# Performance work log

Measured on AMD Instinct MI355X. Metric: run time of the kernel, lower is better.

## Reference

```python
import jax, jax.numpy as jnp
import numpy as np
import math

EPS = 1e-6
N_HEADS = 16
THETA = 10000.0


def rms(x):
    # parameter-free RMSNorm: x * rsqrt(mean(x^2) + eps)
    return x * jax.lax.rsqrt(jnp.mean(x * x, axis=-1, keepdims=True) + EPS)


def silu(x):
    return x * jax.nn.sigmoid(x)


def rope_cos_sin(T, head_dim, theta):
    inv = 1.0 / (theta ** (jnp.arange(0, head_dim, 2, dtype=jnp.float32) / head_dim))
    freqs = jnp.arange(T, dtype=jnp.float32)[:, None] * inv[None, :]  # (T, head_dim/2)
    return jnp.cos(freqs), jnp.sin(freqs)


def apply_rope(x, cos, sin):
    # x: (B, H, T, dh); even/odd interleaved pairs as in torch reshape(...,-1,2).unbind(-1)
    x1 = x[..., 0::2]
    x2 = x[..., 1::2]
    o1 = x1 * cos - x2 * sin
    o2 = x1 * sin + x2 * cos
    return jnp.stack([o1, o2], axis=-1).reshape(x.shape)


def cache_linear(x, down, up):
    # x: (B,T,in), down: (h,in,c), up: (h,out,c) -> (B,T,out)
    a = jnp.einsum('bti,hic->bthc', x, down)
    a = jnp.einsum('bthc,hoc->btho', a, up)
    return rms(jnp.prod(a, axis=2))


def setup_inputs() -> dict:
    key = jax.random.key(0)
    ks = jax.random.split(key, 10)
    B, T, D = 1, 2048, 1024
    d_ff, ncb, cdim = 4096, 4, 64
    lin_std = math.sqrt(2.0 / (D + D))
    return {
        'x': jax.random.normal(ks[0], (B, T, D), jnp.float32),
        'ln1_w': jnp.ones((D,), jnp.float32),
        'ln2_w': jnp.ones((D,), jnp.float32),
        'wq': jax.random.normal(ks[1], (D, D), jnp.float32) * lin_std,
        'wk': jax.random.normal(ks[2], (D, D), jnp.float32) * lin_std,
        'wv': jax.random.normal(ks[3], (D, D), jnp.float32) * lin_std,
        'wo': jax.random.normal(ks[4], (D, D), jnp.float32) * lin_std,
        'w1_down': jax.random.normal(ks[5], (ncb, D, cdim), jnp.float32) * math.sqrt(2.0 / (D + cdim)),
        'w1_up': jax.random.normal(ks[6], (ncb, d_ff, cdim), jnp.float32) * math.sqrt(2.0 / (d_ff + cdim)),
        'w2_down': jax.random.normal(ks[7], (ncb, d_ff, cdim), jnp.float32) * math.sqrt(2.0 / (d_ff + cdim)),
        'w2_up': jax.random.normal(ks[8], (ncb, D, cdim), jnp.float32) * math.sqrt(2.0 / (D + cdim)),
    }


def reference(x, ln1_w, ln2_w, wq, wk, wv, wo, w1_down, w1_up, w2_down, w2_up):
    B, T, D = x.shape
    H = N_HEADS
    dh = D // H

    # --- attention sublayer (pre-RMSNorm) ---
    h = rms(x) * ln1_w
    def proj(w):
        return (h @ w.T).reshape(B, T, H, dh).transpose(0, 2, 1, 3)  # (B,H,T,dh)
    q, k, v = proj(wq), proj(wk), proj(wv)

    cos, sin = rope_cos_sin(T, dh, THETA)  # (T, dh/2)
    q = apply_rope(q, cos, sin)
    k = apply_rope(k, cos, sin)

    scores = jnp.einsum('bhid,bhjd->bhij', q, k) / math.sqrt(dh)
    causal = jnp.tril(jnp.ones((T, T), dtype=bool))
    scores = jnp.where(causal, scores, -jnp.inf)
    attn = jax.nn.softmax(scores, axis=-1)
    o = jnp.einsum('bhij,bhjd->bhid', attn, v)
    o = o.transpose(0, 2, 1, 3).reshape(B, T, D) @ wo.T
    x = x + o

    # --- CacheSiLU FFN sublayer (pre-RMSNorm) ---
    h2 = rms(x) * ln2_w
    a = cache_linear(h2, w1_down, w1_up)   # (B,T,d_ff)
    f = cache_linear(silu(a), w2_down, w2_up)  # (B,T,D)
    return x + f
```

## Files before the change

kernel.cpp:

```cpp
#include <hip/hip_runtime.h>
#include <math.h>
#include <stdint.h>

#define T_LEN   2048
#define D_MODEL 1024
#define NH      16
#define DFF     4096

typedef __attribute__((ext_vector_type(8))) short bf16x8;
typedef __attribute__((ext_vector_type(4))) float f32x4;
typedef __attribute__((ext_vector_type(4))) unsigned short u16x4;
typedef __attribute__((ext_vector_type(8))) unsigned short u16x8;
typedef unsigned short u16;

__device__ inline u16 f2b(float x) {
  unsigned int u = __float_as_uint(x);
  unsigned int r = (u + 0x7fffu + ((u >> 16) & 1u)) >> 16;
  return (u16)r;
}
__device__ inline float b2f(u16 h) { return __uint_as_float(((unsigned int)h) << 16); }

typedef const __attribute__((address_space(1))) unsigned int* gas_t;
typedef __attribute__((address_space(3))) unsigned int* las_t;
__device__ inline void gl_lds16(const void* g, void* l) {
  __builtin_amdgcn_global_load_lds((gas_t)g, (las_t)l, 16, 0, 0);
}

#define MFMA16(a, b, c) __builtin_amdgcn_mfma_f32_16x16x32_bf16((a), (b), (c), 0, 0, 0)
#define VMCNT(N) asm volatile("s_waitcnt vmcnt(" #N ")" ::: "memory")

__global__ __launch_bounds__(256) void prep_conv_kernel(
    const float* s0, const float* s1, const float* s2, const float* s3,
    const float* s4, const float* s5,
    u16* d0, u16* d1, u16* d2, u16* d3, u16* d4, u16* d5) {
  int z = blockIdx.z;
  const float* s; u16* d; int n4;
  switch (z) {
    case 0: s = s0; d = d0; n4 = 262144; break;
    case 1: s = s1; d = d1; n4 = 262144; break;
    case 2: s = s2; d = d2; n4 = 262144; break;
    case 3: s = s3; d = d3; n4 = 262144; break;
    case 4: s = s4; d = d4; n4 = 262144; break;
    default: s = s5; d = d5; n4 = 65536; break;
  }
  int i = blockIdx.x * 256 + threadIdx.x;
  if (i < n4) {
    float4 v = reinterpret_cast<const float4*>(s)[i];
    u16x4 o = {f2b(v.x), f2b(v.y), f2b(v.z), f2b(v.w)};
    reinterpret_cast<u16x4*>(d)[i] = o;
  }
}

__global__ __launch_bounds__(256) void tr_kernel(
    const float* __restrict__ w, u16* __restrict__ wt, int K) {
  int k0 = blockIdx.x * 64, h = blockIdx.y;
  __shared__ float Ts[64][65];
  int tid = threadIdx.x;
#pragma unroll
  for (int i = 0; i < 4; ++i) {
    int idx = tid + i * 256;
    int r = idx >> 4, c4 = (idx & 15) * 4;
    float4 v = *reinterpret_cast<const float4*>(w + ((size_t)h * K + k0 + r) * 64 + c4);
    Ts[r][c4 + 0] = v.x; Ts[r][c4 + 1] = v.y; Ts[r][c4 + 2] = v.z; Ts[r][c4 + 3] = v.w;
  }
  __syncthreads();
#pragma unroll
  for (int i = 0; i < 4; ++i) {
    int idx = tid + i * 256;
    int c = idx >> 4, k4 = (idx & 15) * 4;
    u16x4 o = {f2b(Ts[k4 + 0][c]), f2b(Ts[k4 + 1][c]), f2b(Ts[k4 + 2][c]), f2b(Ts[k4 + 3][c])};
    *reinterpret_cast<u16x4*>(wt + (size_t)(h * 64 + c) * K + k0 + k4) = o;
  }
}

__global__ __launch_bounds__(256) void vtrans_kernel(
    const u16* __restrict__ V, u16* __restrict__ VT) {
  __shared__ u16 Ts[64][72];
  int t0 = blockIdx.x * 64, h = blockIdx.y;
  int tid = threadIdx.x;
#pragma unroll
  for (int it = 0; it < 2; ++it) {
    int c = tid + it * 256;
    int t = c >> 3, d8 = (c & 7) * 8;
    *reinterpret_cast<u16x8*>(&Ts[t][d8]) =
        *reinterpret_cast<const u16x8*>(V + (size_t)(t0 + t) * D_MODEL + h * 64 + d8);
  }
  __syncthreads();
#pragma unroll
  for (int it = 0; it < 2; ++it) {
    int c = tid + it * 256;
    int d = c >> 3, t8 = (c & 7) * 8;
    u16x8 o;
#pragma unroll
    for (int j = 0; j < 8; ++j) o[j] = Ts[t8 + j][d];
    *reinterpret_cast<u16x8*>(VT + ((size_t)h * 64 + d) * T_LEN + t0 + t8) = o;
  }
}

template <int NV, bool WEIGHT>
__global__ __launch_bounds__(256) void rms_bf16_kernel(
    const float* __restrict__ in, const float* __restrict__ w,
    u16* __restrict__ out, int width) {
  int row = blockIdx.x, tid = threadIdx.x;
  const float* rp = in + (size_t)row * width;
  float4 vals[NV];
  float ss = 0.f;
#pragma unroll
  for (int v = 0; v < NV; ++v) {
    vals[v] = reinterpret_cast<const float4*>(rp)[v * 256 + tid];
    ss += vals[v].x * vals[v].x + vals[v].y * vals[v].y +
          vals[v].z * vals[v].z + vals[v].w * vals[v].w;
  }
  for (int off = 32; off; off >>= 1) ss += __shfl_down(ss, off, 64);
  __shared__ float wsum[4];
  if ((tid & 63) == 0) wsum[tid >> 6] = ss;
  __syncthreads();
  float tot = wsum[0] + wsum[1] + wsum[2] + wsum[3];
  float scale = rsqrtf(tot / (float)width + 1e-6f);
#pragma unroll
  for (int v = 0; v < NV; ++v) {
    int c4 = v * 256 + tid;
    float o0 = vals[v].x * scale, o1 = vals[v].y * scale,
          o2 = vals[v].z * scale, o3 = vals[v].w * scale;
    if constexpr (WEIGHT) {
      float4 wv = reinterpret_cast<const float4*>(w)[c4];
      o0 *= wv.x; o1 *= wv.y; o2 *= wv.z; o3 *= wv.w;
    }
    u16x4 ov = {f2b(o0), f2b(o1), f2b(o2), f2b(o3)};
    reinterpret_cast<u16x4*>(out + (size_t)row * width)[c4] = ov;
  }
}

__global__ __launch_bounds__(256) void rms_silu_bf16_kernel(
    const u16* __restrict__ in, u16* __restrict__ out) {
  int row = blockIdx.x, tid = threadIdx.x;
  const u16* rp = in + (size_t)row * DFF;
  float f[16];
  float ss = 0.f;
#pragma unroll
  for (int v = 0; v < 2; ++v) {
    u16x8 c = reinterpret_cast<const u16x8*>(rp)[v * 256 + tid];
#pragma unroll
    for (int j = 0; j < 8; ++j) {
      float x = b2f((u16)c[j]);
      f[v * 8 + j] = x;
      ss += x * x;
    }
  }
  for (int off = 32; off; off >>= 1) ss += __shfl_down(ss, off, 64);
  __shared__ float wsum[4];
  if ((tid & 63) == 0) wsum[tid >> 6] = ss;
  __syncthreads();
  float tot = wsum[0] + wsum[1] + wsum[2] + wsum[3];
  float scale = rsqrtf(tot / (float)DFF + 1e-6f);
#pragma unroll
  for (int v = 0; v < 2; ++v) {
    u16x8 o;
#pragma unroll
    for (int j = 0; j < 8; ++j) {
      float x = f[v * 8 + j] * scale;
      x = x / (1.f + __expf(-x));
      o[j] = f2b(x);
    }
    reinterpret_cast<u16x8*>(out + (size_t)row * DFF)[v * 256 + tid] = o;
  }
}

__global__ __launch_bounds__(256) void rms_add_kernel(
    const float* __restrict__ in, const float* __restrict__ res,
    float* __restrict__ out) {
  int row = blockIdx.x, tid = threadIdx.x;
  float4 v = reinterpret_cast<const float4*>(in + (size_t)row * D_MODEL)[tid];
  float ss = v.x * v.x + v.y * v.y + v.z * v.z + v.w * v.w;
  for (int off = 32; off; off >>= 1) ss += __shfl_down(ss, off, 64);
  __shared__ float wsum[4];
  if ((tid & 63) == 0) wsum[tid >> 6] = ss;
  __syncthreads();
  float tot = wsum[0] + wsum[1] + wsum[2] + wsum[3];
  float scale = rsqrtf(tot / (float)D_MODEL + 1e-6f);
  float4 rv = reinterpret_cast<const float4*>(res + (size_t)row * D_MODEL)[tid];
  float4 o = make_float4(v.x * scale + rv.x, v.y * scale + rv.y,
                         v.z * scale + rv.z, v.w * scale + rv.w);
  reinterpret_cast<float4*>(out + (size_t)row * D_MODEL)[tid] = o;
}

template <int OUT>
__device__ inline void gemm_nt_body(const u16* A, const u16* B, void* Cv,
                                    const float* RES, int N, int lda, int Kloop,
                                    int row0, int col0) {
  __shared__ __align__(16) u16 As[2][128 * 32];
  __shared__ __align__(16) u16 Bs[2][128 * 32];
  int tid = threadIdx.x, lane = tid & 63, wid = tid >> 6;
  int wr = wid >> 1, wc = wid & 1;
  const f32x4 fz = {0.f, 0.f, 0.f, 0.f};
  f32x4 acc[4][4];
#pragma unroll
  for (int m = 0; m < 4; ++m)
#pragma unroll
    for (int n = 0; n < 4; ++n) acc[m][n] = fz;

  auto STAGE = [&](int buf, int k0) {
#pragma unroll
    for (int i = 0; i < 2; ++i) {
      int wl = wid * 2 + i;
      int row = wl * 16 + (lane >> 2);
      int col8 = ((lane & 3) ^ (row & 3)) * 8;
      gl_lds16(A + (size_t)(row0 + row) * lda + k0 + col8, &As[buf][wl * 512]);
      gl_lds16(B + (size_t)(col0 + row) * lda + k0 + col8, &Bs[buf][wl * 512]);
    }
  };

  STAGE(0, 0);
  int nk = Kloop >> 5;
  for (int j = 0; j < nk; ++j) {
    int cur = j & 1;
    if (j + 1 < nk) {
      STAGE(cur ^ 1, (j + 1) * 32);
      VMCNT(4);
    } else {
      VMCNT(0);
    }
    __syncthreads();
    bf16x8 af[4], bfr[4];
#pragma unroll
    for (int m = 0; m < 4; ++m) {
      int r = wr * 64 + m * 16 + (lane & 15);
      af[m] = *reinterpret_cast<const bf16x8*>(
          &As[cur][r * 32 + (((lane >> 4) ^ (r & 3)) << 3)]);
    }
#pragma unroll
    for (int n = 0; n < 4; ++n) {
      int r = wc * 64 + n * 16 + (lane & 15);
      bfr[n] = *reinterpret_cast<const bf16x8*>(
          &Bs[cur][r * 32 + (((lane >> 4) ^ (r & 3)) << 3)]);
    }
#pragma unroll
    for (int m = 0; m < 4; ++m)
#pragma unroll
      for (int n = 0; n < 4; ++n) acc[m][n] = MFMA16(af[m], bfr[n], acc[m][n]);
    __syncthreads();
  }
#pragma unroll
  for (int m = 0; m < 4; ++m)
#pragma unroll
    for (int n = 0; n < 4; ++n)
#pragma unroll
      for (int r = 0; r < 4; ++r) {
        int grow = row0 + wr * 64 + m * 16 + (lane >> 4) * 4 + r;
        int gcol = col0 + wc * 64 + n * 16 + (lane & 15);
        float v = acc[m][n][r];
        if constexpr (OUT == 0) {
          ((u16*)Cv)[(size_t)grow * N + gcol] = f2b(v);
        } else if constexpr (OUT == 1) {
          ((float*)Cv)[(size_t)grow * N + gcol] = v + RES[(size_t)grow * N + gcol];
        } else {
          ((float*)Cv)[(size_t)grow * N + gcol] = v;
        }
      }
}

__global__ __launch_bounds__(256) void gemm_qkv_kernel(
    const u16* __restrict__ A, const u16* Bq, const u16* Bk, const u16* Bv,
    u16* Cq, u16* Ck, u16* Cvp) {
  const u16* B = blockIdx.z == 0 ? Bq : (blockIdx.z == 1 ? Bk : Bv);
  u16* C = blockIdx.z == 0 ? Cq : (blockIdx.z == 1 ? Ck : Cvp);
  gemm_nt_body<0>(A, B, C, nullptr, D_MODEL, D_MODEL, D_MODEL,
                  blockIdx.y * 128, blockIdx.x * 128);
}
__global__ __launch_bounds__(256) void gemm_res_kernel(
    const u16* __restrict__ A, const u16* __restrict__ B, float* __restrict__ C,
    const float* __restrict__ RES) {
  gemm_nt_body<1>(A, B, C, RES, D_MODEL, D_MODEL, D_MODEL,
                  blockIdx.y * 128, blockIdx.x * 128);
}
__global__ __launch_bounds__(256) void gemm_splitk_kernel(
    const u16* __restrict__ A, const u16* __restrict__ B, float* __restrict__ Cp,
    int lda, int Kchunk) {
  int z = blockIdx.z;
  gemm_nt_body<2>(A + (size_t)z * Kchunk, B + (size_t)z * Kchunk,
                  Cp + (size_t)z * (T_LEN * 256), nullptr, 256, lda, Kchunk,
                  blockIdx.y * 128, blockIdx.x * 128);
}
__global__ __launch_bounds__(256) void reduce_conv_kernel(
    const float* __restrict__ part, u16* __restrict__ out, int n4, int nsplit) {
  int i = blockIdx.x * 256 + threadIdx.x;
  if (i >= n4) return;
  float4 a = reinterpret_cast<const float4*>(part)[i];
  for (int s = 1; s < nsplit; ++s) {
    float4 b = reinterpret_cast<const float4*>(part)[i + (size_t)s * n4];
    a.x += b.x; a.y += b.y; a.z += b.z; a.w += b.w;
  }
  u16x4 o = {f2b(a.x), f2b(a.y), f2b(a.z), f2b(a.w)};
  reinterpret_cast<u16x4*>(out)[i] = o;
}

template <bool BF16_OUT>
__global__ __launch_bounds__(256) void cache_up_mfma(
    const u16* __restrict__ Acoef, const u16* __restrict__ UP,
    void* __restrict__ Gv, int N) {
  __shared__ __align__(16) u16 As[2][128 * 64];
  __shared__ __align__(16) u16 Bs[2][128 * 64];
  int tid = threadIdx.x, lane = tid & 63, wid = tid >> 6;
  int wr = wid >> 1, wc = wid & 1;
  int row0 = blockIdx.y * 128, col0 = blockIdx.x * 128;
  const f32x4 fz = {0.f, 0.f, 0.f, 0.f};
  f32x4 prod[4][4];
#pragma unroll
  for (int m = 0; m < 4; ++m)
#pragma unroll
    for (int n = 0; n < 4; ++n) prod[m][n] = fz + 1.f;

  auto STAGE = [&](int buf, int h) {
#pragma unroll
    for (int i = 0; i < 4; ++i) {
      int wl = wid * 4 + i;
      int row = wl * 8 + (lane >> 3);
      int col8 = ((lane & 7) ^ (row & 7)) * 8;
      gl_lds16(Acoef + (size_t)(row0 + row) * 256 + h * 64 + col8, &As[buf][wl * 512]);
      gl_lds16(UP + ((size_t)h * N + col0 + row) * 64 + col8, &Bs[buf][wl * 512]);
    }
  };

  STAGE(0, 0);
  for (int h = 0; h < 4; ++h) {
    int cur = h & 1;
    if (h < 3) {
      STAGE(cur ^ 1, h + 1);
      VMCNT(8);
    } else {
      VMCNT(0);
    }
    __syncthreads();
    f32x4 d[4][4];
#pragma unroll
    for (int m = 0; m < 4; ++m)
#pragma unroll
      for (int n = 0; n < 4; ++n) d[m][n] = fz;
#pragma unroll
    for (int kh = 0; kh < 2; ++kh) {
      bf16x8 af[4], bfr[4];
#pragma unroll
      for (int m = 0; m < 4; ++m) {
        int r = wr * 64 + m * 16 + (lane & 15);
        int slot = kh * 4 + (lane >> 4);
        af[m] = *reinterpret_cast<const bf16x8*>(
            &As[cur][r * 64 + ((slot ^ (r & 7)) << 3)]);
      }
#pragma unroll
      for (int n = 0; n < 4; ++n) {
        int r = wc * 64 + n * 16 + (lane & 15);
        int slot = kh * 4 + (lane >> 4);
        bfr[n] = *reinterpret_cast<const bf16x8*>(
            &Bs[cur][r * 64 + ((slot ^ (r & 7)) << 3)]);
      }
#pragma unroll
      for (int m = 0; m < 4; ++m)
#pragma unroll
        for (int n = 0; n < 4; ++n) d[m][n] = MFMA16(af[m], bfr[n], d[m][n]);
    }
#pragma unroll
    for (int m = 0; m < 4; ++m)
#pragma unroll
      for (int n = 0; n < 4; ++n) prod[m][n] *= d[m][n];
    __syncthreads();
  }
#pragma unroll
  for (int m = 0; m < 4; ++m)
#pragma unroll
    for (int n = 0; n < 4; ++n)
#pragma unroll
      for (int r = 0; r < 4; ++r) {
        int grow = row0 + wr * 64 + m * 16 + (lane >> 4) * 4 + r;
        int gcol = col0 + wc * 64 + n * 16 + (lane & 15);
        if constexpr (BF16_OUT)
          ((u16*)Gv)[(size_t)grow * N + gcol] = f2b(prod[m][n][r]);
        else
          ((float*)Gv)[(size_t)grow * N + gcol] = prod[m][n][r];
      }
}

__global__ __launch_bounds__(256) void rope_bf16_kernel(u16* __restrict__ q,
                                                        u16* __restrict__ k) {
  int t = blockIdx.x, tid = threadIdx.x;
  const float NEG = -0.28782313662425573f;
#pragma unroll
  for (int u = 0; u < 2; ++u) {
    int p = tid + u * 256;
    int i = p & 31;
    int col = (p >> 5) * 64 + 2 * i;
    float ang = (float)t * __expf(NEG * (float)i);
    float sv, cv;
    __sincosf(ang, &sv, &cv);
    size_t idx = (size_t)t * D_MODEL + col;
    unsigned int* qp = reinterpret_cast<unsigned int*>(q + idx);
    unsigned int qv = *qp;
    float q1 = b2f(qv & 0xffff), q2 = b2f(qv >> 16);
    *qp = (unsigned int)f2b(q1 * cv - q2 * sv) |
          ((unsigned int)f2b(q1 * sv + q2 * cv) << 16);
    unsigned int* kp = reinterpret_cast<unsigned int*>(k + idx);
    unsigned int kv = *kp;
    float k1 = b2f(kv & 0xffff), k2 = b2f(kv >> 16);
    *kp = (unsigned int)f2b(k1 * cv - k2 * sv) |
          ((unsigned int)f2b(k1 * sv + k2 * cv) << 16);
  }
}

__global__ __launch_bounds__(256) void attn_mfma_kernel(
    const u16* __restrict__ Q, const u16* __restrict__ Kb,
    const u16* __restrict__ VT, u16* __restrict__ O) {
  __shared__ __align__(16) u16 Ks[2][64 * 64];
  __shared__ __align__(16) u16 Vt[2][64 * 64];
  int tid = threadIdx.x, lane = tid & 63, wid = tid >> 6;
  int G = lane >> 4, ql = lane & 15;
  int head = blockIdx.y, hoff = head * 64;
  int qt = (int)gridDim.x - 1 - (int)blockIdx.x;
  int q0 = qt * 64;
  int qg = q0 + wid * 16 + ql;

  bf16x8 aq[2];
  {
    const u16* qp = Q + (size_t)qg * D_MODEL + hoff + G * 8;
    aq[0] = *reinterpret_cast<const bf16x8*>(qp);
    aq[1] = *reinterpret_cast<const bf16x8*>(qp + 32);
  }
  const f32x4 fz = {0.f, 0.f, 0.f, 0.f};
  f32x4 accO[4];
#pragma unroll
  for (int n = 0; n < 4; ++n) accO[n] = fz;
  float m_p = -INFINITY, l_p = 0.f;

  auto STAGE = [&](int buf, int j0) {
#pragma unroll
    for (int i = 0; i < 2; ++i) {
      int wl = wid * 2 + i;
      int row = wl * 8 + (lane >> 3);
      int col8 = ((lane & 7) ^ (row & 7)) * 8;
      gl_lds16(Kb + (size_t)(j0 + row) * D_MODEL + hoff + col8, &Ks[buf][wl * 512]);
      gl_lds16(VT + ((size_t)hoff + row) * T_LEN + j0 + col8, &Vt[buf][wl * 512]);
    }
  };

  int ntile = qt + 1;
  STAGE(0, 0);
  for (int jt = 0; jt < ntile; ++jt) {
    int j0 = jt * 64;
    int cur = jt & 1;
    if (jt + 1 < ntile) {
      STAGE(cur ^ 1, j0 + 64);
      VMCNT(4);
    } else {
      VMCNT(0);
    }
    __syncthreads();
    f32x4 s[4];
#pragma unroll
    for (int n = 0; n < 4; ++n) s[n] = fz;
#pragma unroll
    for (int n = 0; n < 4; ++n) {
      int kr = n * 16 + ql;
#pragma unroll
      for (int h = 0; h < 2; ++h) {
        int slot = (h * 4 + G) ^ (kr & 7);
        bf16x8 bk = *reinterpret_cast<const bf16x8*>(&Ks[cur][kr * 64 + slot * 8]);
        s[n] = MFMA16(bk, aq[h], s[n]);
      }
    }
    bool diag = (jt == ntile - 1);
#pragma unroll
    for (int n = 0; n < 4; ++n)
#pragma unroll
      for (int r = 0; r < 4; ++r) {
        float sv = s[n][r] * 0.125f;
        if (diag && (j0 + n * 16 + 4 * G + r > qg)) sv = -INFINITY;
        s[n][r] = sv;
      }
    float mx = s[0][0];
#pragma unroll
    for (int n = 0; n < 4; ++n)
#pragma unroll
      for (int r = 0; r < 4; ++r) mx = fmaxf(mx, s[n][r]);
    mx = fmaxf(mx, __shfl_xor(mx, 16, 64));
    mx = fmaxf(mx, __shfl_xor(mx, 32, 64));
    float mn = fmaxf(m_p, mx);
    float rsc = __expf(m_p - mn);
    m_p = mn;
    float ls = 0.f;
#pragma unroll
    for (int n = 0; n < 4; ++n)
#pragma unroll
      for (int r = 0; r < 4; ++r) {
        float p = __expf(s[n][r] - mn);
        s[n][r] = p;
        ls += p;
      }
    ls += __shfl_xor(ls, 16, 64);
    ls += __shfl_xor(ls, 32, 64);
    l_p = l_p * rsc + ls;
    unsigned int w32[4][2];
#pragma unroll
    for (int n = 0; n < 4; ++n)
#pragma unroll
      for (int rr = 0; rr < 2; ++rr) {
        unsigned int pk;
        asm("v_cvt_pk_bf16_f32 %0, %1, %2"
            : "=v"(pk) : "v"(s[n][2 * rr]), "v"(s[n][2 * rr + 1]));
        w32[n][rr] = pk;
      }
    float rscx[4];
#pragma unroll
    for (int r = 0; r < 4; ++r) rscx[r] = __shfl(rsc, 4 * G + r, 64);
#pragma unroll
    for (int n = 0; n < 4; ++n)
#pragma unroll
      for (int r = 0; r < 4; ++r) accO[n][r] *= rscx[r];
#pragma unroll
    for (int kh = 0; kh < 2; ++kh) {
      union { unsigned int w[4]; bf16x8 v; } ap;
#pragma unroll
      for (int w = 0; w < 4; ++w) {
        int src = ql + (((2 * G + (w >> 1)) & 3) << 4);
        unsigned int v0 = (unsigned int)__shfl((int)w32[2 * kh][w & 1], src, 64);
        unsigned int v1 = (unsigned int)__shfl((int)w32[2 * kh + 1][w & 1], src, 64);
        ap.w[w] = (G >> 1) ? v1 : v0;
      }
#pragma unroll
      for (int n = 0; n < 4; ++n) {
        int d = n * 16 + ql;
        int slot = (kh * 4 + G) ^ (d & 7);
        bf16x8 bv = *reinterpret_cast<const bf16x8*>(&Vt[cur][d * 64 + slot * 8]);
        accO[n] = MFMA16(ap.v, bv, accO[n]);
      }
    }
    __syncthreads();
  }
  float invl = 1.f / l_p;
  float linvx[4];
#pragma unroll
  for (int r = 0; r < 4; ++r) linvx[r] = __shfl(invl, 4 * G + r, 64);
#pragma unroll
  for (int n = 0; n < 4; ++n)
#pragma unroll
    for (int r = 0; r < 4; ++r) {
      int qrow = q0 + wid * 16 + 4 * G + r;
      O[(size_t)qrow * D_MODEL + hoff + n * 16 + ql] = f2b(accO[n][r] * linvx[r]);
    }
}

extern "C" void kernel_launch(void* const* d_in, const int* in_sizes, int n_in,
                              void* d_out, int out_size, void* d_ws, size_t ws_size,
                              hipStream_t stream) {
  (void)in_sizes; (void)n_in; (void)out_size; (void)ws_size;
  const float* x   = (const float*)d_in[0];
  const float* ln1 = (const float*)d_in[1];
  const float* ln2 = (const float*)d_in[2];
  const float* wq  = (const float*)d_in[3];
  const float* wk  = (const float*)d_in[4];
  const float* wv  = (const float*)d_in[5];
  const float* wo  = (const float*)d_in[6];
  const float* w1d = (const float*)d_in[7];
  const float* w1u = (const float*)d_in[8];
  const float* w2d = (const float*)d_in[9];
  const float* w2u = (const float*)d_in[10];
  float* out = (float*)d_out;
  char* ws = (char*)d_ws;
  const size_t HMB = 1ull << 19;

  u16*   wqb  = (u16*)(ws + 0 * HMB);
  u16*   wkb  = (u16*)(ws + 4 * HMB);
  u16*   wvb  = (u16*)(ws + 8 * HMB);
  u16*   wob  = (u16*)(ws + 12 * HMB);
  u16*   w1ub = (u16*)(ws + 16 * HMB);
  u16*   w2ub = (u16*)(ws + 20 * HMB);
  u16*   wt1  = (u16*)(ws + 21 * HMB);
  u16*   wt2  = (u16*)(ws + 22 * HMB);
  u16*   hb   = (u16*)(ws + 26 * HMB);
  float* x1   = (float*)(ws + 34 * HMB);
  u16*   abuf = (u16*)(ws + 50 * HMB);
  u16*   qb   = (u16*)(ws + 52 * HMB);
  u16*   kb   = (u16*)(ws + 60 * HMB);
  u16*   vb   = (u16*)(ws + 68 * HMB);
  u16*   vtb  = (u16*)(ws + 76 * HMB);
  u16*   aob  = (u16*)(ws + 84 * HMB);
  u16*   g    = (u16*)(ws + 52 * HMB);
  float* g2   = (float*)(ws + 52 * HMB);
  u16*   sb   = (u16*)(ws + 84 * HMB);
  float* part = (float*)(ws + 116 * HMB);

  dim3 b256(256);
  prep_conv_kernel<<<dim3(1024, 1, 6), b256, 0, stream>>>(
      wq, wk, wv, wo, w1u, w2u, wqb, wkb, wvb, wob, w1ub, w2ub);
  tr_kernel<<<dim3(16, 4), b256, 0, stream>>>(w1d, wt1, 1024);
  tr_kernel<<<dim3(64, 4), b256, 0, stream>>>(w2d, wt2, 4096);
  rms_bf16_kernel<1, true><<<T_LEN, b256, 0, stream>>>(x, ln1, hb, 1024);
  gemm_qkv_kernel<<<dim3(8, 16, 3), b256, 0, stream>>>(hb, wqb, wkb, wvb, qb, kb, vb);
  rope_bf16_kernel<<<T_LEN, b256, 0, stream>>>(qb, kb);
  vtrans_kernel<<<dim3(32, 16), b256, 0, stream>>>(vb, vtb);
  attn_mfma_kernel<<<dim3(T_LEN / 64, NH), b256, 0, stream>>>(qb, kb, vtb, aob);
  gemm_res_kernel<<<dim3(8, 16), b256, 0, stream>>>(aob, wob, x1, x);
  rms_bf16_kernel<1, true><<<T_LEN, b256, 0, stream>>>(x1, ln2, hb, 1024);
  gemm_splitk_kernel<<<dim3(2, 16, 4), b256, 0, stream>>>(hb, wt1, part, 1024, 256);
  reduce_conv_kernel<<<512, b256, 0, stream>>>(part, abuf, 131072, 4);
  cache_up_mfma<true><<<dim3(32, 16), b256, 0, stream>>>(abuf, w1ub, g, 4096);
  rms_silu_bf16_kernel<<<T_LEN, b256, 0, stream>>>(g, sb);
  gemm_splitk_kernel<<<dim3(2, 16, 8), b256, 0, stream>>>(sb, wt2, part, 4096, 512);
  reduce_conv_kernel<<<512, b256, 0, stream>>>(part, abuf, 131072, 8);
  cache_up_mfma<false><<<dim3(8, 16), b256, 0, stream>>>(abuf, w2ub, g2, 1024);
  rms_add_kernel<<<T_LEN, b256, 0, stream>>>(g2, x1, out);
}
```

Baseline: 283.8 us.

## Split causal attention over KV chunks and merge partials in a combine kernel

The attention kernel now splits the KV range into chunks of 8 tiles along a third grid dimension. Each block writes an unnormalized bf16 partial output plus its running max and sum, and a new combine kernel merges the chunks with log-sum-exp weights. This is meant to fix load imbalance and low parallelism from long causal rows (32x16 blocks with up to 32 tiles each), at the cost of an extra launch, partial-output traffic, and bf16 rounding of the unnormalized partials. The softmax max and sum reductions are also rebalanced into trees, with a clamp to guard against fully masked chunks.

Result: no change. 283.2 us (-0.2%).

```diff
diff --git a/kernel.cpp b/kernel.cpp
--- a/kernel.cpp
+++ b/kernel.cpp
@@ -405,15 +405,18 @@
   }
 }
 
+#define KVCHUNK_TILES 8
 __global__ __launch_bounds__(256) void attn_mfma_kernel(
     const u16* __restrict__ Q, const u16* __restrict__ Kb,
-    const u16* __restrict__ VT, u16* __restrict__ O) {
+    const u16* __restrict__ VT, u16* __restrict__ Opart,
+    float* __restrict__ mlb) {
+  int qt = blockIdx.x, c = blockIdx.z;
+  if (c * KVCHUNK_TILES > qt) return;
   __shared__ __align__(16) u16 Ks[2][64 * 64];
   __shared__ __align__(16) u16 Vt[2][64 * 64];
   int tid = threadIdx.x, lane = tid & 63, wid = tid >> 6;
   int G = lane >> 4, ql = lane & 15;
   int head = blockIdx.y, hoff = head * 64;
-  int qt = (int)gridDim.x - 1 - (int)blockIdx.x;
   int q0 = qt * 64;
   int qg = q0 + wid * 16 + ql;
 
@@ -440,12 +443,15 @@
     }
   };
 
-  int ntile = qt + 1;
-  STAGE(0, 0);
-  for (int jt = 0; jt < ntile; ++jt) {
+  int t0 = c * KVCHUNK_TILES;
+  int tend = min(t0 + KVCHUNK_TILES, qt + 1);
+  int ntile = tend - t0;
+  STAGE(0, t0 * 64);
+  for (int jl = 0; jl < ntile; ++jl) {
+    int jt = t0 + jl;
     int j0 = jt * 64;
-    int cur = jt & 1;
-    if (jt + 1 < ntile) {
+    int cur = jl & 1;
+    if (jl + 1 < ntile) {
       STAGE(cur ^ 1, j0 + 64);
       VMCNT(4);
     } else {
@@ -465,7 +471,7 @@
         s[n] = MFMA16(bk, aq[h], s[n]);
       }
     }
-    bool diag = (jt == ntile - 1);
+    bool diag = (jt == qt);
 #pragma unroll
     for (int n = 0; n < 4; ++n)
 #pragma unroll
@@ -474,25 +480,25 @@
         if (diag && (j0 + n * 16 + 4 * G + r > qg)) sv = -INFINITY;
         s[n][r] = sv;
       }
-    float mx = s[0][0];
+    float m4[4];
 #pragma unroll
     for (int n = 0; n < 4; ++n)
-#pragma unroll
-      for (int r = 0; r < 4; ++r) mx = fmaxf(mx, s[n][r]);
+      m4[n] = fmaxf(fmaxf(s[n][0], s[n][1]), fmaxf(s[n][2], s[n][3]));
+    float mx = fmaxf(fmaxf(m4[0], m4[1]), fmaxf(m4[2], m4[3]));
     mx = fmaxf(mx, __shfl_xor(mx, 16, 64));
     mx = fmaxf(mx, __shfl_xor(mx, 32, 64));
     float mn = fmaxf(m_p, mx);
-    float rsc = __expf(m_p - mn);
+    float sub = fmaxf(mn, -1e30f);
+    float rsc = __expf(m_p - sub);
     m_p = mn;
-    float ls = 0.f;
-#pragma unroll
-    for (int n = 0; n < 4; ++n)
-#pragma unroll
-      for (int r = 0; r < 4; ++r) {
-        float p = __expf(s[n][r] - mn);
-        s[n][r] = p;
-        ls += p;
-      }
+    float s4[4];
+#pragma unroll
+    for (int n = 0; n < 4; ++n) {
+#pragma unroll
+      for (int r = 0; r < 4; ++r) s[n][r] = __expf(s[n][r] - sub);
+      s4[n] = (s[n][0] + s[n][1]) + (s[n][2] + s[n][3]);
+    }
+    float ls = (s4[0] + s4[1]) + (s4[2] + s4[3]);
     ls += __shfl_xor(ls, 16, 64);
     ls += __shfl_xor(ls, 32, 64);
     l_p = l_p * rsc + ls;
@@ -533,17 +539,46 @@
     }
     __syncthreads();
   }
-  float invl = 1.f / l_p;
-  float linvx[4];
-#pragma unroll
-  for (int r = 0; r < 4; ++r) linvx[r] = __shfl(invl, 4 * G + r, 64);
 #pragma unroll
   for (int n = 0; n < 4; ++n)
 #pragma unroll
     for (int r = 0; r < 4; ++r) {
       int qrow = q0 + wid * 16 + 4 * G + r;
-      O[(size_t)qrow * D_MODEL + hoff + n * 16 + ql] = f2b(accO[n][r] * linvx[r]);
-    }
+      Opart[((size_t)c * T_LEN + qrow) * D_MODEL + hoff + n * 16 + ql] =
+          f2b(accO[n][r]);
+    }
+  if (G == 0) {
+    int qrow = q0 + wid * 16 + ql;
+    mlb[(c * NH + head) * T_LEN + qrow] = m_p;
+    mlb[4 * NH * T_LEN + (c * NH + head) * T_LEN + qrow] = l_p;
+  }
+}
+
+__global__ __launch_bounds__(256) void attn_combine_kernel(
+    const u16* __restrict__ Opart, const float* __restrict__ mlb,
+    u16* __restrict__ O) {
+  int t = blockIdx.x, tid = threadIdx.x;
+  int head = tid >> 4, d4 = (tid & 15) * 4;
+  int nc = t / (KVCHUNK_TILES * 64) + 1;
+  float mv[4];
+  float ms = -INFINITY;
+  for (int c = 0; c < nc; ++c) {
+    mv[c] = mlb[(c * NH + head) * T_LEN + t];
+    ms = fmaxf(ms, mv[c]);
+  }
+  float lsum = 0.f;
+  float o0 = 0.f, o1 = 0.f, o2 = 0.f, o3 = 0.f;
+  for (int c = 0; c < nc; ++c) {
+    float w = __expf(mv[c] - ms);
+    lsum += w * mlb[4 * NH * T_LEN + (c * NH + head) * T_LEN + t];
+    u16x4 op = *reinterpret_cast<const u16x4*>(
+        Opart + ((size_t)c * T_LEN + t) * D_MODEL + head * 64 + d4);
+    o0 += w * b2f(op[0]); o1 += w * b2f(op[1]);
+    o2 += w * b2f(op[2]); o3 += w * b2f(op[3]);
+  }
+  float inv = 1.f / lsum;
+  u16x4 ov = {f2b(o0 * inv), f2b(o1 * inv), f2b(o2 * inv), f2b(o3 * inv)};
+  *reinterpret_cast<u16x4*>(O + (size_t)t * D_MODEL + head * 64 + d4) = ov;
 }
 
 extern "C" void kernel_launch(void* const* d_in, const int* in_sizes, int n_in,
@@ -585,6 +620,8 @@
   float* g2   = (float*)(ws + 52 * HMB);
   u16*   sb   = (u16*)(ws + 84 * HMB);
   float* part = (float*)(ws + 116 * HMB);
+  u16*   opart= (u16*)(ws + 116 * HMB);
+  float* mlb  = (float*)(ws + 148 * HMB);
 
   dim3 b256(256);
   prep_conv_kernel<<<dim3(1024, 1, 6), b256, 0, stream>>>(
@@ -595,7 +632,9 @@
   gemm_qkv_kernel<<<dim3(8, 16, 3), b256, 0, stream>>>(hb, wqb, wkb, wvb, qb, kb, vb);
   rope_bf16_kernel<<<T_LEN, b256, 0, stream>>>(qb, kb);
   vtrans_kernel<<<dim3(32, 16), b256, 0, stream>>>(vb, vtb);
-  attn_mfma_kernel<<<dim3(T_LEN / 64, NH), b256, 0, stream>>>(qb, kb, vtb, aob);
+  attn_mfma_kernel<<<dim3(T_LEN / 64, NH, 4), b256, 0, stream>>>(qb, kb, vtb,
+                                                                 opart, mlb);
+  attn_combine_kernel<<<T_LEN, b256, 0, stream>>>(opart, mlb, aob);
   gemm_res_kernel<<<dim3(8, 16), b256, 0, stream>>>(aob, wob, x1, x);
   rms_bf16_kernel<1, true><<<T_LEN, b256, 0, stream>>>(x1, ln2, hb, 1024);
   gemm_splitk_kernel<<<dim3(2, 16, 4), b256, 0, stream>>>(hb, wt1, part, 1024, 256);
```
